# Kernel tuning notes

Hardware: AMD Instinct MI355X
Metric: run time of the kernel (lower is better)

The kernel has to match this reference:

```python
import jax, jax.numpy as jnp
import numpy as np

K = 16          # per-chain hidden states: int(sqrt(args.hidden_dim=256))
K2 = K * K      # joint enumerated state (w, x)
SCALE = 1.0     # handlers.scale(scale=args.scale)


def setup_inputs() -> dict:
    key = jax.random.key(0)
    ks = jax.random.split(key, 8)
    N, T, D, B = 4096, 512, 88, 1024
    # Bernoulli observations (binary piano-roll style data)
    sequences = (jax.random.uniform(ks[0], (N, T, D)) < 0.3).astype(jnp.float32)
    lengths = jax.random.randint(ks[1], (N,), T // 4, T + 1).astype(jnp.int32)
    mb = jax.random.randint(ks[2], (B,), 0, N).astype(jnp.int32)
    mask = jnp.ones((B,), dtype=bool)

    def simplex(k, shape):
        p = jax.random.uniform(k, shape) + 0.1
        return p / p.sum(-1, keepdims=True)

    probs_w = simplex(ks[3], (K, K))
    probs_x = simplex(ks[4], (K, K))
    w_init = simplex(ks[5], (K,))
    x_init = simplex(ks[6], (K,))
    probs_y = jax.random.uniform(ks[7], (K, K, D), minval=0.05, maxval=0.95)
    return dict(sequences=sequences, probs_w=probs_w, probs_x=probs_x,
                w_init=w_init, x_init=x_init, probs_y=probs_y,
                lengths=lengths, mb=mb, mask=mask)


def reference(sequences, probs_w, probs_x, w_init, x_init, probs_y, lengths, mb, mask):
    """Exact marginal log-likelihood of the factorial HMM (what parallel
    enumeration over w_t, x_t computes): forward algorithm over the joint
    256-state chain with factorized transitions and Bernoulli emissions."""
    T = sequences.shape[1]
    seq = sequences[mb]          # [B, T, D]
    len_mb = lengths[mb]         # [B]

    # Bernoulli emission log-probs, contracted over tones plate (dim -1):
    # logB[t, b, k] = sum_d [ y*log(p) + (1-y)*log(1-p) ],  k = (w, x) flat
    logp = jnp.log(probs_y).reshape(K2, -1)       # [K2, D]
    log1mp = jnp.log1p(-probs_y).reshape(K2, -1)  # [K2, D]
    logB = jnp.einsum('btd,kd->tbk', seq, logp - log1mp) + log1mp.sum(-1)  # [T,B,K2]

    # Factorized joint transition: logT[(w,x),(w',x')] = log p(w'|w) + log p(x'|x)
    logT = (jnp.log(probs_w)[:, None, :, None] +
            jnp.log(probs_x)[None, :, None, :]).reshape(K2, K2)
    log_init = (jnp.log(w_init)[:, None] + jnp.log(x_init)[None, :]).reshape(K2)

    alpha0 = log_init + logB[0]  # [B, K2]; all lengths >= 1 here

    def step(alpha, inp):
        logb_t, t = inp
        nxt = jax.nn.logsumexp(alpha[:, :, None] + logT[None], axis=1) + logb_t
        valid = (t < len_mb)[:, None]            # mask: t < lengths[mb]
        return jnp.where(valid, nxt, alpha), None

    alpha, _ = jax.lax.scan(step, alpha0, (logB[1:], jnp.arange(1, T)))
    loglik = jax.nn.logsumexp(alpha, axis=-1)    # [B]
    return SCALE * jnp.sum(jnp.where(mask, loglik, 0.0))
```

## Files before the change

### kernel.cpp

```cpp
#include <hip/hip_runtime.h>


typedef _Float16 h4 __attribute__((ext_vector_type(4)));
typedef _Float16 h8 __attribute__((ext_vector_type(8)));
typedef float v4f __attribute__((ext_vector_type(4)));

#define TT 512
#define DD 88
#define NB 1024
#define LOG4096 8.317766167f

#define WS_E    0ull
#define WS_M    268435456ull
#define WS_BF   (WS_M + 2097152ull)
#define WS_BIAS (WS_BF + 49152ull)
#define WS_WF   (WS_BIAS + 1024ull)
#define WS_XF   (WS_WF + 512ull)

__device__ inline float dpp_wave_sum(float x) {
  union fi { float f; int i; };
  fi v; v.f = x;
#define DPPADD(ctrl, rmask)                                              \
  { fi t; t.i = __builtin_amdgcn_update_dpp(0, v.i, ctrl, rmask, 0xf, false); \
    v.f += t.f; }
  DPPADD(0x111, 0xf)
  DPPADD(0x112, 0xf)
  DPPADD(0x114, 0xf)
  DPPADD(0x118, 0xf)
  DPPADD(0x142, 0xa)
  DPPADD(0x143, 0xc)
#undef DPPADD
  fi o; o.i = __builtin_amdgcn_readlane(v.i, 63);
  return o.f;
}

__global__ __launch_bounds__(256) void prep_kernel(
    const float* __restrict__ pw, const float* __restrict__ px,
    const float* __restrict__ py, float* __restrict__ out,
    unsigned char* __restrict__ ws) {
  int tid = threadIdx.x;
  int blk = blockIdx.x;
  _Float16* bfrag = (_Float16*)(ws + WS_BF);
  float* bias = (float*)(ws + WS_BIAS);
  _Float16* wf = (_Float16*)(ws + WS_WF);
  _Float16* xf = (_Float16*)(ws + WS_XF);
  if (blk == 0) {
    float s = 0.f;
    for (int d = 0; d < DD; ++d) s += __logf(1.0f - py[tid * DD + d]);
    bias[tid] = s;
  } else if (blk == 1) {
    if (tid == 0) out[0] = 0.0f;
    if (tid < 64) {
      int q = tid >> 4, c = tid & 15;
      #pragma unroll
      for (int i = 0; i < 4; ++i) {
        wf[tid * 4 + i] = (_Float16)pw[(4 * q + i) * 16 + c];
        xf[tid * 4 + i] = (_Float16)px[(4 * q + i) * 16 + c];
      }
    }
  } else {
    int idx = (blk - 2) * 256 + tid;
    int j = idx & 7, l = (idx >> 3) & 63, n = (idx >> 9) & 15, c = idx >> 13;
    int state = n * 16 + (l & 15);
    int d = c * 32 + (l >> 4) * 8 + j;
    float v = 0.f;
    if (d < DD) {
      float p = py[state * DD + d];
      v = __logf(p) - __logf(1.0f - p);
    }
    bfrag[idx] = (_Float16)v;
  }
}

__global__ __launch_bounds__(256) void emis_kernel(
    const float* __restrict__ seq, const int* __restrict__ lengths,
    const int* __restrict__ mb, unsigned char* __restrict__ ws) {
  int b = blockIdx.x >> 3;
  int blk8 = blockIdx.x & 7;
  int item = mb[b];
  int len = lengths[item];
  if (blk8 * 64 >= len) return;
  __shared__ uint4 lbf[3072];
  __shared__ float lbias[256];
  int tid = threadIdx.x;
  const uint4* gbf = (const uint4*)(ws + WS_BF);
  #pragma unroll
  for (int i = 0; i < 12; ++i) lbf[tid + 256 * i] = gbf[tid + 256 * i];
  lbias[tid] = ((const float*)(ws + WS_BIAS))[tid];
  __syncthreads();
  int wave = tid >> 6, lane = tid & 63;
  int t0 = (blk8 * 4 + wave) * 16;
  if (t0 >= len) return;
  int q = lane >> 4, cc = lane & 15;
  const float* srow = seq + ((size_t)item * TT + (t0 + cc)) * DD;
  h8 af[3];
  #pragma unroll
  for (int c = 0; c < 3; ++c) {
    int d0 = c * 32 + q * 8;
    h8 a;
    if (d0 < DD) {
      float4 f0 = *(const float4*)(srow + d0);
      float4 f1 = *(const float4*)(srow + d0 + 4);
      a[0] = (_Float16)f0.x; a[1] = (_Float16)f0.y;
      a[2] = (_Float16)f0.z; a[3] = (_Float16)f0.w;
      a[4] = (_Float16)f1.x; a[5] = (_Float16)f1.y;
      a[6] = (_Float16)f1.z; a[7] = (_Float16)f1.w;
    } else {
      #pragma unroll
      for (int j = 0; j < 8; ++j) a[j] = (_Float16)0.f;
    }
    af[c] = a;
  }
  v4f acc[16];
  #pragma unroll
  for (int n = 0; n < 16; ++n) acc[n] = (v4f){0.f, 0.f, 0.f, 0.f};
  #pragma unroll
  for (int n = 0; n < 16; ++n) {
    #pragma unroll
    for (int c = 0; c < 3; ++c) {
      union { uint4 u; h8 h; } bf;
      bf.u = lbf[(c * 16 + n) * 64 + lane];
      acc[n] = __builtin_amdgcn_mfma_f32_16x16x32_f16(af[c], bf.h, acc[n], 0, 0, 0);
    }
  }
  #pragma unroll
  for (int n = 0; n < 16; ++n) {
    float bn = lbias[16 * n + cc];
    acc[n][0] += bn; acc[n][1] += bn; acc[n][2] += bn; acc[n][3] += bn;
  }
  float mrow[4];
  #pragma unroll
  for (int r = 0; r < 4; ++r) {
    float mv = acc[0][r];
    #pragma unroll
    for (int n = 1; n < 16; ++n) mv = fmaxf(mv, acc[n][r]);
    mv = fmaxf(mv, __shfl_xor(mv, 1));
    mv = fmaxf(mv, __shfl_xor(mv, 2));
    mv = fmaxf(mv, __shfl_xor(mv, 4));
    mv = fmaxf(mv, __shfl_xor(mv, 8));
    mrow[r] = mv;
  }
  float* marr = (float*)(ws + WS_M);
  if (cc == 0) {
    float4 mm;
    mm.x = mrow[0]; mm.y = mrow[1]; mm.z = mrow[2]; mm.w = mrow[3];
    *(float4*)(marr + b * TT + t0 + 4 * q) = mm;
  }
  _Float16* E = (_Float16*)(ws + WS_E);
  #pragma unroll
  for (int r = 0; r < 4; ++r) {
    int tt = t0 + 4 * q + r;
    union { _Float16 h[16]; uint4 u[2]; } pk;
    #pragma unroll
    for (int n = 0; n < 16; ++n)
      pk.h[n] = (_Float16)__expf(acc[n][r] - mrow[r]);
    uint4* dst = (uint4*)(E + ((size_t)b * TT + tt) * 256 + cc * 16);
    dst[0] = pk.u[0];
    dst[1] = pk.u[1];
  }
}

#define LOADCH(EA, MA, tbase)                                          \
  {                                                                    \
    _Pragma("unroll") for (int i2 = 0; i2 < 16; ++i2) {                \
      int tt = (tbase) + i2;                                           \
      tt = tt < (TT - 1) ? tt : (TT - 1);                              \
      EA[i2] = *(const uint2*)(Eb + ((size_t)tt << 8) + off);          \
      MA[i2] = M[tt];                                                  \
    }                                                                  \
  }

#define STEPCH(EA, MA)                                                 \
  {                                                                    \
    _Pragma("unroll") for (int i2 = 0; i2 < 16; ++i2) {                \
      if (t >= len) { done = true; break; }                            \
      float rl = (float)sv[0] + (float)sv[1] +                         \
                 (float)sv[2] + (float)sv[3];                          \
      float Rn = dpp_wave_sum(rl);                                     \
      v4f zz = (v4f){0.f, 0.f, 0.f, 0.f};                              \
      v4f d1 = __builtin_amdgcn_mfma_f32_16x16x16f16(sv, Wf, zz, 0, 0, 0); \
      h4 a2;                                                           \
      { auto lo = __builtin_amdgcn_cvt_pkrtz(d1[0], d1[1]);            \
        auto hi = __builtin_amdgcn_cvt_pkrtz(d1[2], d1[3]);            \
        a2[0] = lo[0]; a2[1] = lo[1]; a2[2] = hi[0]; a2[3] = hi[1]; }  \
      v4f d2 = __builtin_amdgcn_mfma_f32_16x16x16f16(a2, Xf, zz, 0, 0, 0); \
      union { uint2 u; h4 h; } bt;                                     \
      bt.u = EA[i2];                                                   \
      h4 pm;                                                           \
      { auto lo = __builtin_amdgcn_cvt_pkrtz(d2[0], d2[1]);            \
        auto hi = __builtin_amdgcn_cvt_pkrtz(d2[2], d2[3]);            \
        pm[0] = lo[0]; pm[1] = lo[1]; pm[2] = hi[0]; pm[3] = hi[1]; }  \
      pm = pm * bt.h;                                                  \
      float fsc = __builtin_amdgcn_rcpf(Rn) * 4096.0f;                 \
      _Float16 fh = (_Float16)fsc;                                     \
      h4 fv; fv[0] = fh; fv[1] = fh; fv[2] = fh; fv[3] = fh;           \
      sv = pm * fv;                                                    \
      logacc += __logf(Rn) + MA[i2] - LOG4096;                         \
      ++t;                                                             \
    }                                                                  \
  }

__global__ __launch_bounds__(64) void fwd_kernel(
    const int* __restrict__ lengths, const int* __restrict__ mb,
    const float* __restrict__ w_init, const float* __restrict__ x_init,
    float* __restrict__ out, const unsigned char* __restrict__ ws) {
  int b = blockIdx.x;
  int lane = threadIdx.x;
  int q = lane >> 4, cc = lane & 15;
  int item = mb[b];
  int len = lengths[item];
  const _Float16* Eb = (const _Float16*)(ws + WS_E) + (size_t)b * (TT * 256);
  const float* M = (const float*)(ws + WS_M) + b * TT;
  union { uint2 u; h4 h; } wfu, xfu;
  wfu.u = *(const uint2*)((const _Float16*)(ws + WS_WF) + lane * 4);
  xfu.u = *(const uint2*)((const _Float16*)(ws + WS_XF) + lane * 4);
  h4 Wf = wfu.h, Xf = xfu.h;
  int off = cc * 16 + 4 * q;
  union { uint2 u; h4 h; } bt0;
  bt0.u = *(const uint2*)(Eb + off);
  float xiv = x_init[cc] * 4096.0f;
  h4 sv;
  sv[0] = (_Float16)(w_init[4 * q + 0] * xiv * (float)bt0.h[0]);
  sv[1] = (_Float16)(w_init[4 * q + 1] * xiv * (float)bt0.h[1]);
  sv[2] = (_Float16)(w_init[4 * q + 2] * xiv * (float)bt0.h[2]);
  sv[3] = (_Float16)(w_init[4 * q + 3] * xiv * (float)bt0.h[3]);
  float logacc = M[0] - LOG4096;
  uint2 eA[16], eB[16];
  float mA[16], mB[16];
  LOADCH(eA, mA, 1);
  LOADCH(eB, mB, 17);
  int t = 1;
  int nextbase = 33;
  bool done = (len <= 1);
  while (!done) {
    STEPCH(eA, mA);
    if (done) break;
    LOADCH(eA, mA, nextbase);
    nextbase += 16;
    STEPCH(eB, mB);
    if (done) break;
    LOADCH(eB, mB, nextbase);
    nextbase += 16;
  }
  float Sf = dpp_wave_sum((float)sv[0] + (float)sv[1] +
                          (float)sv[2] + (float)sv[3]);
  float ll = logacc + __logf(Sf);
  if (lane == 0) atomicAdd(out, ll);
}

extern "C" void kernel_launch(void* const* d_in, const int* in_sizes, int n_in,
                              void* d_out, int out_size, void* d_ws, size_t ws_size,
                              hipStream_t stream) {
  const float* seq = (const float*)d_in[0];
  const float* pw = (const float*)d_in[1];
  const float* px = (const float*)d_in[2];
  const float* wi = (const float*)d_in[3];
  const float* xi = (const float*)d_in[4];
  const float* py = (const float*)d_in[5];
  const int* lengths = (const int*)d_in[6];
  const int* mb = (const int*)d_in[7];
  float* out = (float*)d_out;
  unsigned char* ws = (unsigned char*)d_ws;

  prep_kernel<<<98, 256, 0, stream>>>(pw, px, py, out, ws);
  emis_kernel<<<NB * 8, 256, 0, stream>>>(seq, lengths, mb, ws);
  fwd_kernel<<<NB, 64, 0, stream>>>(lengths, mb, wi, xi, out, ws);
}
```

Measured before the change: 1.022 ms.

## Fuse emission computation into forward recursion kernel via per-chunk LDS staging

Merges the emission MFMA kernel and the forward-recursion kernel into one 64-thread-per-sequence kernel. Each 16-timestep chunk's emissions are computed with MFMA from prefetched sequence rows, exponentiated, and staged in LDS, then consumed by the recursion. This removes the large fp16 emission buffer write and reread in global memory. In exchange, only 1024 single-wave blocks now do all the emission matmul work serially alongside the latency-bound recursion, and 48 uint4 B-fragments are held in registers per lane.

```diff
diff --git a/kernel.cpp b/kernel.cpp
--- a/kernel.cpp
+++ b/kernel.cpp
@@ -10,10 +10,8 @@
 #define NB 1024
 #define LOG4096 8.317766167f
 
-#define WS_E    0ull
-#define WS_M    268435456ull
-#define WS_BF   (WS_M + 2097152ull)
-#define WS_BIAS (WS_BF + 49152ull)
+#define WS_BF   0ull
+#define WS_BIAS 49152ull
 #define WS_WF   (WS_BIAS + 1024ull)
 #define WS_XF   (WS_WF + 512ull)
 
@@ -72,176 +70,177 @@
   }
 }
 
-__global__ __launch_bounds__(256) void emis_kernel(
+__global__ __launch_bounds__(64, 1) void fused_kernel(
     const float* __restrict__ seq, const int* __restrict__ lengths,
-    const int* __restrict__ mb, unsigned char* __restrict__ ws) {
-  int b = blockIdx.x >> 3;
-  int blk8 = blockIdx.x & 7;
-  int item = mb[b];
-  int len = lengths[item];
-  if (blk8 * 64 >= len) return;
-  __shared__ uint4 lbf[3072];
-  __shared__ float lbias[256];
-  int tid = threadIdx.x;
-  const uint4* gbf = (const uint4*)(ws + WS_BF);
-  #pragma unroll
-  for (int i = 0; i < 12; ++i) lbf[tid + 256 * i] = gbf[tid + 256 * i];
-  lbias[tid] = ((const float*)(ws + WS_BIAS))[tid];
-  __syncthreads();
-  int wave = tid >> 6, lane = tid & 63;
-  int t0 = (blk8 * 4 + wave) * 16;
-  if (t0 >= len) return;
+    const int* __restrict__ mb, const float* __restrict__ w_init,
+    const float* __restrict__ x_init, float* __restrict__ out,
+    const unsigned char* __restrict__ ws) {
+  __shared__ _Float16 bt_s[16 * 264];
+  __shared__ float m_s[16];
+  int b = blockIdx.x, lane = threadIdx.x;
   int q = lane >> 4, cc = lane & 15;
-  const float* srow = seq + ((size_t)item * TT + (t0 + cc)) * DD;
-  h8 af[3];
-  #pragma unroll
-  for (int c = 0; c < 3; ++c) {
-    int d0 = c * 32 + q * 8;
-    h8 a;
-    if (d0 < DD) {
-      float4 f0 = *(const float4*)(srow + d0);
-      float4 f1 = *(const float4*)(srow + d0 + 4);
-      a[0] = (_Float16)f0.x; a[1] = (_Float16)f0.y;
-      a[2] = (_Float16)f0.z; a[3] = (_Float16)f0.w;
-      a[4] = (_Float16)f1.x; a[5] = (_Float16)f1.y;
-      a[6] = (_Float16)f1.z; a[7] = (_Float16)f1.w;
-    } else {
-      #pragma unroll
-      for (int j = 0; j < 8; ++j) a[j] = (_Float16)0.f;
-    }
-    af[c] = a;
-  }
-  v4f acc[16];
-  #pragma unroll
-  for (int n = 0; n < 16; ++n) acc[n] = (v4f){0.f, 0.f, 0.f, 0.f};
-  #pragma unroll
-  for (int n = 0; n < 16; ++n) {
-    #pragma unroll
-    for (int c = 0; c < 3; ++c) {
-      union { uint4 u; h8 h; } bf;
-      bf.u = lbf[(c * 16 + n) * 64 + lane];
-      acc[n] = __builtin_amdgcn_mfma_f32_16x16x32_f16(af[c], bf.h, acc[n], 0, 0, 0);
-    }
-  }
-  #pragma unroll
-  for (int n = 0; n < 16; ++n) {
-    float bn = lbias[16 * n + cc];
-    acc[n][0] += bn; acc[n][1] += bn; acc[n][2] += bn; acc[n][3] += bn;
-  }
-  float mrow[4];
-  #pragma unroll
-  for (int r = 0; r < 4; ++r) {
-    float mv = acc[0][r];
-    #pragma unroll
-    for (int n = 1; n < 16; ++n) mv = fmaxf(mv, acc[n][r]);
-    mv = fmaxf(mv, __shfl_xor(mv, 1));
-    mv = fmaxf(mv, __shfl_xor(mv, 2));
-    mv = fmaxf(mv, __shfl_xor(mv, 4));
-    mv = fmaxf(mv, __shfl_xor(mv, 8));
-    mrow[r] = mv;
-  }
-  float* marr = (float*)(ws + WS_M);
-  if (cc == 0) {
-    float4 mm;
-    mm.x = mrow[0]; mm.y = mrow[1]; mm.z = mrow[2]; mm.w = mrow[3];
-    *(float4*)(marr + b * TT + t0 + 4 * q) = mm;
-  }
-  _Float16* E = (_Float16*)(ws + WS_E);
-  #pragma unroll
-  for (int r = 0; r < 4; ++r) {
-    int tt = t0 + 4 * q + r;
-    union { _Float16 h[16]; uint4 u[2]; } pk;
-    #pragma unroll
-    for (int n = 0; n < 16; ++n)
-      pk.h[n] = (_Float16)__expf(acc[n][r] - mrow[r]);
-    uint4* dst = (uint4*)(E + ((size_t)b * TT + tt) * 256 + cc * 16);
-    dst[0] = pk.u[0];
-    dst[1] = pk.u[1];
-  }
-}
-
-#define LOADCH(EA, MA, tbase)                                          \
-  {                                                                    \
-    _Pragma("unroll") for (int i2 = 0; i2 < 16; ++i2) {                \
-      int tt = (tbase) + i2;                                           \
-      tt = tt < (TT - 1) ? tt : (TT - 1);                              \
-      EA[i2] = *(const uint2*)(Eb + ((size_t)tt << 8) + off);          \
-      MA[i2] = M[tt];                                                  \
-    }                                                                  \
-  }
-
-#define STEPCH(EA, MA)                                                 \
-  {                                                                    \
-    _Pragma("unroll") for (int i2 = 0; i2 < 16; ++i2) {                \
-      if (t >= len) { done = true; break; }                            \
-      float rl = (float)sv[0] + (float)sv[1] +                         \
-                 (float)sv[2] + (float)sv[3];                          \
-      float Rn = dpp_wave_sum(rl);                                     \
-      v4f zz = (v4f){0.f, 0.f, 0.f, 0.f};                              \
-      v4f d1 = __builtin_amdgcn_mfma_f32_16x16x16f16(sv, Wf, zz, 0, 0, 0); \
-      h4 a2;                                                           \
-      { auto lo = __builtin_amdgcn_cvt_pkrtz(d1[0], d1[1]);            \
-        auto hi = __builtin_amdgcn_cvt_pkrtz(d1[2], d1[3]);            \
-        a2[0] = lo[0]; a2[1] = lo[1]; a2[2] = hi[0]; a2[3] = hi[1]; }  \
-      v4f d2 = __builtin_amdgcn_mfma_f32_16x16x16f16(a2, Xf, zz, 0, 0, 0); \
-      union { uint2 u; h4 h; } bt;                                     \
-      bt.u = EA[i2];                                                   \
-      h4 pm;                                                           \
-      { auto lo = __builtin_amdgcn_cvt_pkrtz(d2[0], d2[1]);            \
-        auto hi = __builtin_amdgcn_cvt_pkrtz(d2[2], d2[3]);            \
-        pm[0] = lo[0]; pm[1] = lo[1]; pm[2] = hi[0]; pm[3] = hi[1]; }  \
-      pm = pm * bt.h;                                                  \
-      float fsc = __builtin_amdgcn_rcpf(Rn) * 4096.0f;                 \
-      _Float16 fh = (_Float16)fsc;                                     \
-      h4 fv; fv[0] = fh; fv[1] = fh; fv[2] = fh; fv[3] = fh;           \
-      sv = pm * fv;                                                    \
-      logacc += __logf(Rn) + MA[i2] - LOG4096;                         \
-      ++t;                                                             \
-    }                                                                  \
-  }
-
-__global__ __launch_bounds__(64) void fwd_kernel(
-    const int* __restrict__ lengths, const int* __restrict__ mb,
-    const float* __restrict__ w_init, const float* __restrict__ x_init,
-    float* __restrict__ out, const unsigned char* __restrict__ ws) {
-  int b = blockIdx.x;
-  int lane = threadIdx.x;
-  int q = lane >> 4, cc = lane & 15;
-  int item = mb[b];
-  int len = lengths[item];
-  const _Float16* Eb = (const _Float16*)(ws + WS_E) + (size_t)b * (TT * 256);
-  const float* M = (const float*)(ws + WS_M) + b * TT;
+  int item = mb[b], len = lengths[item];
+  int nch = (len + 15) >> 4;
+
   union { uint2 u; h4 h; } wfu, xfu;
   wfu.u = *(const uint2*)((const _Float16*)(ws + WS_WF) + lane * 4);
   xfu.u = *(const uint2*)((const _Float16*)(ws + WS_XF) + lane * 4);
   h4 Wf = wfu.h, Xf = xfu.h;
-  int off = cc * 16 + 4 * q;
-  union { uint2 u; h4 h; } bt0;
-  bt0.u = *(const uint2*)(Eb + off);
-  float xiv = x_init[cc] * 4096.0f;
+
+  uint4 bf[48];
+  const uint4* gbf = (const uint4*)(ws + WS_BF);
+  #pragma unroll
+  for (int i = 0; i < 48; ++i) bf[i] = gbf[i * 64 + lane];
+
+  const float* bias = (const float*)(ws + WS_BIAS);
+  float biasr[16];
+  #pragma unroll
+  for (int n = 0; n < 16; ++n) biasr[n] = bias[16 * n + cc];
+
+  const float* sbase = seq + (size_t)item * TT * DD;
+
+  float4 pf[6];
+  {
+    const float* srow = sbase + (size_t)cc * DD;
+    #pragma unroll
+    for (int ci = 0; ci < 3; ++ci) {
+      int d0 = ci * 32 + q * 8;
+      if (d0 < DD) {
+        pf[2 * ci]     = *(const float4*)(srow + d0);
+        pf[2 * ci + 1] = *(const float4*)(srow + d0 + 4);
+      }
+    }
+  }
+
   h4 sv;
-  sv[0] = (_Float16)(w_init[4 * q + 0] * xiv * (float)bt0.h[0]);
-  sv[1] = (_Float16)(w_init[4 * q + 1] * xiv * (float)bt0.h[1]);
-  sv[2] = (_Float16)(w_init[4 * q + 2] * xiv * (float)bt0.h[2]);
-  sv[3] = (_Float16)(w_init[4 * q + 3] * xiv * (float)bt0.h[3]);
-  float logacc = M[0] - LOG4096;
-  uint2 eA[16], eB[16];
-  float mA[16], mB[16];
-  LOADCH(eA, mA, 1);
-  LOADCH(eB, mB, 17);
-  int t = 1;
-  int nextbase = 33;
-  bool done = (len <= 1);
-  while (!done) {
-    STEPCH(eA, mA);
-    if (done) break;
-    LOADCH(eA, mA, nextbase);
-    nextbase += 16;
-    STEPCH(eB, mB);
-    if (done) break;
-    LOADCH(eB, mB, nextbase);
-    nextbase += 16;
+  sv[0] = (_Float16)0.f; sv[1] = (_Float16)0.f;
+  sv[2] = (_Float16)0.f; sv[3] = (_Float16)0.f;
+  float logacc = 0.f;
+  int t = 0;
+  bool done = false;
+  int toff = cc * 16 + 4 * q;
+
+  for (int c = 0; c < nch; ++c) {
+    h8 af[3];
+    #pragma unroll
+    for (int ci = 0; ci < 3; ++ci) {
+      h8 a;
+      int d0 = ci * 32 + q * 8;
+      if (d0 < DD) {
+        float4 f0 = pf[2 * ci], f1 = pf[2 * ci + 1];
+        a[0] = (_Float16)f0.x; a[1] = (_Float16)f0.y;
+        a[2] = (_Float16)f0.z; a[3] = (_Float16)f0.w;
+        a[4] = (_Float16)f1.x; a[5] = (_Float16)f1.y;
+        a[6] = (_Float16)f1.z; a[7] = (_Float16)f1.w;
+      } else {
+        #pragma unroll
+        for (int j = 0; j < 8; ++j) a[j] = (_Float16)0.f;
+      }
+      af[ci] = a;
+    }
+    {
+      int cp = (c + 1 < nch) ? c + 1 : nch - 1;
+      const float* srow = sbase + (size_t)(16 * cp + cc) * DD;
+      #pragma unroll
+      for (int ci = 0; ci < 3; ++ci) {
+        int d0 = ci * 32 + q * 8;
+        if (d0 < DD) {
+          pf[2 * ci]     = *(const float4*)(srow + d0);
+          pf[2 * ci + 1] = *(const float4*)(srow + d0 + 4);
+        }
+      }
+    }
+    v4f acc[16];
+    #pragma unroll
+    for (int n = 0; n < 16; ++n) {
+      v4f a0 = (v4f){0.f, 0.f, 0.f, 0.f};
+      #pragma unroll
+      for (int ci = 0; ci < 3; ++ci) {
+        union { uint4 u; h8 h; } bfh;
+        bfh.u = bf[ci * 16 + n];
+        a0 = __builtin_amdgcn_mfma_f32_16x16x32_f16(af[ci], bfh.h, a0, 0, 0, 0);
+      }
+      acc[n] = a0;
+    }
+    #pragma unroll
+    for (int n = 0; n < 16; ++n) {
+      float bn = biasr[n];
+      acc[n][0] += bn; acc[n][1] += bn; acc[n][2] += bn; acc[n][3] += bn;
+    }
+    float mrow[4];
+    #pragma unroll
+    for (int r = 0; r < 4; ++r) {
+      float mv = acc[0][r];
+      #pragma unroll
+      for (int n = 1; n < 16; ++n) mv = fmaxf(mv, acc[n][r]);
+      mv = fmaxf(mv, __shfl_xor(mv, 1));
+      mv = fmaxf(mv, __shfl_xor(mv, 2));
+      mv = fmaxf(mv, __shfl_xor(mv, 4));
+      mv = fmaxf(mv, __shfl_xor(mv, 8));
+      mrow[r] = mv;
+    }
+    if (cc == 0) {
+      #pragma unroll
+      for (int r = 0; r < 4; ++r) m_s[4 * q + r] = mrow[r];
+    }
+    #pragma unroll
+    for (int r = 0; r < 4; ++r) {
+      union { _Float16 h[16]; uint4 u[2]; } pk;
+      #pragma unroll
+      for (int n = 0; n < 16; ++n)
+        pk.h[n] = (_Float16)__expf(acc[n][r] - mrow[r]);
+      _Float16* dst = bt_s + (4 * q + r) * 264 + cc * 16;
+      *(uint4*)(dst) = pk.u[0];
+      *(uint4*)(dst + 8) = pk.u[1];
+    }
+
+    if (c == 0) {
+      union { uint2 u; h4 h; } bt0;
+      bt0.u = *(const uint2*)(bt_s + toff);
+      float xiv = x_init[cc] * 4096.0f;
+      sv[0] = (_Float16)(w_init[4 * q + 0] * xiv * (float)bt0.h[0]);
+      sv[1] = (_Float16)(w_init[4 * q + 1] * xiv * (float)bt0.h[1]);
+      sv[2] = (_Float16)(w_init[4 * q + 2] * xiv * (float)bt0.h[2]);
+      sv[3] = (_Float16)(w_init[4 * q + 3] * xiv * (float)bt0.h[3]);
+      logacc = m_s[0] - LOG4096;
+      t = 1;
+      done = (len <= 1);
+    }
+    int i0 = (c == 0) ? 1 : 0;
+    #pragma unroll
+    for (int i2 = 0; i2 < 16; ++i2) {
+      if (i2 >= i0 && !done) {
+        if (t >= len) {
+          done = true;
+        } else {
+          float rl = (float)sv[0] + (float)sv[1] +
+                     (float)sv[2] + (float)sv[3];
+          float Rn = dpp_wave_sum(rl);
+          v4f zz = (v4f){0.f, 0.f, 0.f, 0.f};
+          v4f d1 = __builtin_amdgcn_mfma_f32_16x16x16f16(sv, Wf, zz, 0, 0, 0);
+          h4 a2;
+          { auto lo = __builtin_amdgcn_cvt_pkrtz(d1[0], d1[1]);
+            auto hi = __builtin_amdgcn_cvt_pkrtz(d1[2], d1[3]);
+            a2[0] = lo[0]; a2[1] = lo[1]; a2[2] = hi[0]; a2[3] = hi[1]; }
+          v4f d2 = __builtin_amdgcn_mfma_f32_16x16x16f16(a2, Xf, zz, 0, 0, 0);
+          union { uint2 u; h4 h; } bt;
+          bt.u = *(const uint2*)(bt_s + i2 * 264 + toff);
+          h4 pm;
+          { auto lo = __builtin_amdgcn_cvt_pkrtz(d2[0], d2[1]);
+            auto hi = __builtin_amdgcn_cvt_pkrtz(d2[2], d2[3]);
+            pm[0] = lo[0]; pm[1] = lo[1]; pm[2] = hi[0]; pm[3] = hi[1]; }
+          pm = pm * bt.h;
+          float fsc = __builtin_amdgcn_rcpf(Rn) * 4096.0f;
+          _Float16 fh = (_Float16)fsc;
+          h4 fv; fv[0] = fh; fv[1] = fh; fv[2] = fh; fv[3] = fh;
+          sv = pm * fv;
+          logacc += __logf(Rn) + m_s[i2] - LOG4096;
+          ++t;
+        }
+      }
+    }
   }
+
   float Sf = dpp_wave_sum((float)sv[0] + (float)sv[1] +
                           (float)sv[2] + (float)sv[3]);
   float ll = logacc + __logf(Sf);
@@ -263,6 +262,5 @@
   unsigned char* ws = (unsigned char*)d_ws;
 
   prep_kernel<<<98, 256, 0, stream>>>(pw, px, py, out, ws);
-  emis_kernel<<<NB * 8, 256, 0, stream>>>(seq, lengths, mb, ws);
-  fwd_kernel<<<NB, 64, 0, stream>>>(lengths, mb, wi, xi, out, ws);
-}
+  fused_kernel<<<NB, 64, 0, stream>>>(seq, lengths, mb, wi, xi, out, ws);
+}
```

Measured after the change: 939.1 us. -8.1%, faster.
